# Kernel tuning notes

Measured on AMD Instinct MI355X. Metric: run time of the kernel, lower is better.

## Reference

```python
import jax, jax.numpy as jnp
import numpy as np

BS = 2
EMBED = 256
NH = 8
NL = 4
NP = 4
HD = EMBED // NH
SHAPES = [(128, 128), (64, 64), (32, 32), (16, 16)]
NQ = sum(h * w for h, w in SHAPES)  # 21760


def setup_inputs() -> dict:
    key = jax.random.key(0)
    ks = jax.random.split(key, 12)
    s = 1.0 / np.sqrt(EMBED)
    return {
        "query": jax.random.normal(ks[0], (BS, NQ, EMBED), jnp.float32),
        "reference_points": jax.random.uniform(ks[1], (BS, NQ, NL, 2), jnp.float32),
        "value": jax.random.normal(ks[2], (BS, NQ, EMBED), jnp.float32),
        "W_off": jax.random.normal(ks[3], (EMBED, NH * NL * NP * 2), jnp.float32) * 0.01,
        "b_off": jax.random.normal(ks[4], (NH * NL * NP * 2,), jnp.float32) * 0.5,
        "W_attn": jax.random.normal(ks[5], (EMBED, NH * NL * NP), jnp.float32) * 0.02,
        "b_attn": jnp.zeros((NH * NL * NP,), jnp.float32),
        "W_v": jax.random.normal(ks[6], (EMBED, EMBED), jnp.float32) * s,
        "b_v": jnp.zeros((EMBED,), jnp.float32),
        "W_out": jax.random.normal(ks[7], (EMBED, EMBED), jnp.float32) * s,
        "b_out": jnp.zeros((EMBED,), jnp.float32),
        "value_spatial_shapes": np.asarray(SHAPES, dtype=np.int64),
    }


def _ms_deform_attn(value, shapes, loc, aw):
    # value: [bs,V,nh,d]; loc: [bs,nq,nh,L,P,2] in [0,1]; aw: [bs,nq,nh,L,P]
    bs, V, nh, d = value.shape
    nq = loc.shape[1]
    out = jnp.zeros((bs, nq, nh, d), value.dtype)
    start = 0
    b_idx = jnp.arange(bs)[:, None, None, None]
    h_idx = jnp.arange(nh)[None, None, :, None]
    for l, (H, W) in enumerate(shapes):
        H, W = int(H), int(W)
        v = value[:, start:start + H * W].reshape(bs, H, W, nh, d)
        start += H * W
        g = 2.0 * loc[:, :, :, l] - 1.0  # [bs,nq,nh,P,2], grid_sample convention
        # align_corners=False pixel coordinates
        x = ((g[..., 0] + 1.0) * W - 1.0) * 0.5
        y = ((g[..., 1] + 1.0) * H - 1.0) * 0.5
        x0 = jnp.floor(x); y0 = jnp.floor(y)
        wx1 = x - x0; wx0 = 1.0 - wx1
        wy1 = y - y0; wy0 = 1.0 - wy1

        def gather(yi, xi):
            inb = (yi >= 0) & (yi < H) & (xi >= 0) & (xi < W)
            yc = jnp.clip(yi, 0, H - 1).astype(jnp.int32)
            xc = jnp.clip(xi, 0, W - 1).astype(jnp.int32)
            vals = v[b_idx, yc, xc, h_idx]  # [bs,nq,nh,P,d]
            return vals * inb[..., None].astype(v.dtype)

        samp = (gather(y0, x0) * (wy0 * wx0)[..., None]
                + gather(y0, x0 + 1) * (wy0 * wx1)[..., None]
                + gather(y0 + 1, x0) * (wy1 * wx0)[..., None]
                + gather(y0 + 1, x0 + 1) * (wy1 * wx1)[..., None])
        out = out + jnp.einsum('bqhpd,bqhp->bqhd', samp, aw[:, :, :, l])
    return out.reshape(bs, nq, nh * d)


def reference(query, reference_points, value, W_off, b_off, W_attn, b_attn,
              W_v, b_v, W_out, b_out, value_spatial_shapes):
    shapes = np.asarray(value_spatial_shapes)  # static [L,2]
    bs, nq, _ = query.shape
    v = (value @ W_v + b_v).reshape(bs, -1, NH, HD)
    off = (query @ W_off + b_off).reshape(bs, nq, NH, NL, NP, 2)
    aw = (query @ W_attn + b_attn).reshape(bs, nq, NH, NL * NP)
    aw = jax.nn.softmax(aw, axis=-1).reshape(bs, nq, NH, NL, NP)
    # offset normalizer: (W,H) per level
    norm = jnp.asarray(shapes[:, ::-1].astype(np.float32))  # [L,2]
    loc = reference_points[:, :, None, :, None, :] + off / norm[None, None, None, :, None, :]
    out = _ms_deform_attn(v, shapes, loc, aw)
    return out @ W_out + b_out
```

## Files before the change

### kernel.cpp

```cpp
#include <hip/hip_runtime.h>
#include <math.h>

#define BS 2
#define NQ 21760
#define V_LEN 21760
#define EMBED 256
#define NH 8
#define NL 4
#define NP 4
#define HD 32

typedef __bf16 bf16;
typedef __bf16 bf16x8 __attribute__((ext_vector_type(8)));
typedef __bf16 bf16x4 __attribute__((ext_vector_type(4)));
typedef float f32x4 __attribute__((ext_vector_type(4)));

__global__ __launch_bounds__(256) void cast_wt(const float* __restrict__ W,
                                               bf16* __restrict__ WT, int N)
{
    int id = blockIdx.x * 256 + threadIdx.x;
    int n = id >> 8, k = id & 255;
    WT[id] = (bf16)W[k * N + n];
}

__global__ __launch_bounds__(384) void concat_bias(const float* __restrict__ b_off,
                                                   const float* __restrict__ b_attn,
                                                   float* __restrict__ bc)
{
    int id = threadIdx.x;
    bc[id] = (id < 256) ? b_off[id] : b_attn[id - 256];
}

template<bool A_BF16, bool OUT_BF16>
__global__ __launch_bounds__(256) void gemm_mfma(
    const void* __restrict__ Av, const bf16* __restrict__ WT,
    const float* __restrict__ bias, void* __restrict__ Cv,
    int N, int K, int ntn)
{
    const int bnt = blockIdx.x % ntn;
    const int bmt = blockIdx.x / ntn;
    const int bm = bmt * 128, bn = bnt * 128;

    __shared__ __align__(16) bf16 As[128][40];
    __shared__ __align__(16) bf16 Bs[128][40];

    const int tid = threadIdx.x;
    const int lane = tid & 63, wv = tid >> 6;
    const int wr = wv >> 1, wc = wv & 1;
    const int quad = lane >> 4, l16 = lane & 15;

    f32x4 acc[4][4];
    #pragma unroll
    for (int i = 0; i < 4; i++)
        #pragma unroll
        for (int j = 0; j < 4; j++)
            acc[i][j] = (f32x4){0.f, 0.f, 0.f, 0.f};

    for (int k0 = 0; k0 < K; k0 += 32) {
        if constexpr (A_BF16) {
            const bf16* A = (const bf16*)Av;
            #pragma unroll
            for (int i = 0; i < 2; i++) {
                int row = (tid >> 2) + i * 64, seg = tid & 3;
                bf16x8 v = *(const bf16x8*)&A[(size_t)(bm + row) * K + k0 + seg * 8];
                *(bf16x8*)&As[row][seg * 8] = v;
            }
        } else {
            const float* A = (const float*)Av;
            #pragma unroll
            for (int i = 0; i < 4; i++) {
                int row = (tid >> 3) + i * 32, f4 = tid & 7;
                float4 f = *(const float4*)&A[(size_t)(bm + row) * K + k0 + f4 * 4];
                bf16x4 h;
                h[0] = (bf16)f.x; h[1] = (bf16)f.y; h[2] = (bf16)f.z; h[3] = (bf16)f.w;
                *(bf16x4*)&As[row][f4 * 4] = h;
            }
        }
        #pragma unroll
        for (int i = 0; i < 2; i++) {
            int row = (tid >> 2) + i * 64, seg = tid & 3;
            bf16x8 v = *(const bf16x8*)&WT[(size_t)(bn + row) * K + k0 + seg * 8];
            *(bf16x8*)&Bs[row][seg * 8] = v;
        }
        __syncthreads();

        bf16x8 af[4], bfr[4];
        #pragma unroll
        for (int mi = 0; mi < 4; mi++)
            af[mi] = *(const bf16x8*)&As[wr * 64 + mi * 16 + l16][quad * 8];
        #pragma unroll
        for (int ni = 0; ni < 4; ni++)
            bfr[ni] = *(const bf16x8*)&Bs[wc * 64 + ni * 16 + l16][quad * 8];
        #pragma unroll
        for (int mi = 0; mi < 4; mi++)
            #pragma unroll
            for (int ni = 0; ni < 4; ni++)
                acc[mi][ni] = __builtin_amdgcn_mfma_f32_16x16x32_bf16(
                    af[mi], bfr[ni], acc[mi][ni], 0, 0, 0);
        __syncthreads();
    }

    #pragma unroll
    for (int mi = 0; mi < 4; mi++) {
        #pragma unroll
        for (int ni = 0; ni < 4; ni++) {
            const int col = bn + wc * 64 + ni * 16 + l16;
            const int row0 = bm + wr * 64 + mi * 16 + quad * 4;
            const float bc = bias[col];
            #pragma unroll
            for (int r = 0; r < 4; r++) {
                float v = acc[mi][ni][r] + bc;
                if constexpr (OUT_BF16)
                    ((bf16*)Cv)[(size_t)(row0 + r) * N + col] = (bf16)v;
                else
                    ((float*)Cv)[(size_t)(row0 + r) * N + col] = v;
            }
        }
    }
}

__global__ __launch_bounds__(64) void deform_sample(
    const bf16* __restrict__ vproj, const float* __restrict__ offaw,
    const float* __restrict__ refp, bf16* __restrict__ sampled)
{
    const int q = blockIdx.x;
    const int b = blockIdx.y;
    const int bq = b * NQ + q;
    const int t = threadIdx.x;

    __shared__ float s_off[256];
    __shared__ float s_aw[128];
    __shared__ __align__(16) float s_w[128][4];
    __shared__ __align__(16) int   s_idx[128][4];

    const float* row = offaw + (size_t)bq * 384;
    #pragma unroll
    for (int i = 0; i < 4; i++) s_off[t + i * 64] = row[t + i * 64];
    #pragma unroll
    for (int i = 0; i < 2; i++) s_aw[t + i * 64] = row[256 + t + i * 64];
    __syncthreads();

    if (t < 8) {
        float m = -1e30f;
        #pragma unroll
        for (int i = 0; i < 16; i++) m = fmaxf(m, s_aw[t * 16 + i]);
        float ssum = 0.f;
        #pragma unroll
        for (int i = 0; i < 16; i++) {
            float e = __expf(s_aw[t * 16 + i] - m);
            s_aw[t * 16 + i] = e;
            ssum += e;
        }
        float r = 1.0f / ssum;
        #pragma unroll
        for (int i = 0; i < 16; i++) s_aw[t * 16 + i] *= r;
    }
    __syncthreads();

    #pragma unroll
    for (int sI = 0; sI < 2; sI++) {
        int s = t + sI * 64;
        int h = s >> 4, lp = s & 15, l = lp >> 2, p = lp & 3;
        int Wl = 128 >> l, Hl = 128 >> l;
        int st = (l == 0) ? 0 : (l == 1) ? 16384 : (l == 2) ? 20480 : 21504;
        float rx = refp[((size_t)bq * 4 + l) * 2 + 0];
        float ry = refp[((size_t)bq * 4 + l) * 2 + 1];
        float ox = s_off[((h * NL + l) * NP + p) * 2 + 0];
        float oy = s_off[((h * NL + l) * NP + p) * 2 + 1];
        float fW = (float)Wl, fH = (float)Hl;
        float x = (rx + ox / fW) * fW - 0.5f;
        float y = (ry + oy / fH) * fH - 0.5f;
        float xf = floorf(x), yf = floorf(y);
        int x0 = (int)xf, y0 = (int)yf;
        float wx1 = x - xf, wx0 = 1.f - wx1;
        float wy1 = y - yf, wy0 = 1.f - wy1;
        float aw = s_aw[h * 16 + lp];
        bool vx0 = (x0 >= 0) && (x0 < Wl);
        bool vx1 = (x0 + 1 >= 0) && (x0 + 1 < Wl);
        bool vy0 = (y0 >= 0) && (y0 < Hl);
        bool vy1 = (y0 + 1 >= 0) && (y0 + 1 < Hl);
        int cx0 = min(max(x0, 0), Wl - 1), cx1 = min(max(x0 + 1, 0), Wl - 1);
        int cy0 = min(max(y0, 0), Hl - 1), cy1 = min(max(y0 + 1, 0), Hl - 1);
        int d = lp * 8 + h;
        s_idx[d][0] = st + cy0 * Wl + cx0;  s_w[d][0] = (vy0 && vx0) ? wy0 * wx0 * aw : 0.f;
        s_idx[d][1] = st + cy0 * Wl + cx1;  s_w[d][1] = (vy0 && vx1) ? wy0 * wx1 * aw : 0.f;
        s_idx[d][2] = st + cy1 * Wl + cx0;  s_w[d][2] = (vy1 && vx0) ? wy1 * wx0 * aw : 0.f;
        s_idx[d][3] = st + cy1 * Wl + cx1;  s_w[d][3] = (vy1 && vx1) ? wy1 * wx1 * aw : 0.f;
    }
    __syncthreads();

    const int h = t >> 3;
    const int choff = t * 4;
    const bf16* vbc = vproj + (size_t)b * V_LEN * EMBED + choff;
    float a0 = 0.f, a1 = 0.f, a2 = 0.f, a3 = 0.f;
    #pragma unroll 4
    for (int lp = 0; lp < 16; lp++) {
        const int d = lp * 8 + h;
        const float4 w4 = *(const float4*)&s_w[d][0];
        const int4  i4 = *(const int4*)&s_idx[d][0];
        bf16x4 v0 = *(const bf16x4*)(vbc + (i4.x << 8));
        bf16x4 v1 = *(const bf16x4*)(vbc + (i4.y << 8));
        bf16x4 v2 = *(const bf16x4*)(vbc + (i4.z << 8));
        bf16x4 v3 = *(const bf16x4*)(vbc + (i4.w << 8));
        a0 += w4.x * (float)v0[0] + w4.y * (float)v1[0] + w4.z * (float)v2[0] + w4.w * (float)v3[0];
        a1 += w4.x * (float)v0[1] + w4.y * (float)v1[1] + w4.z * (float)v2[1] + w4.w * (float)v3[1];
        a2 += w4.x * (float)v0[2] + w4.y * (float)v1[2] + w4.z * (float)v2[2] + w4.w * (float)v3[2];
        a3 += w4.x * (float)v0[3] + w4.y * (float)v1[3] + w4.z * (float)v2[3] + w4.w * (float)v3[3];
    }

    bf16x4 o;
    o[0] = (bf16)a0; o[1] = (bf16)a1; o[2] = (bf16)a2; o[3] = (bf16)a3;
    *(bf16x4*)&sampled[(size_t)bq * 256 + choff] = o;
}

extern "C" void kernel_launch(void* const* d_in, const int* in_sizes, int n_in,
                              void* d_out, int out_size, void* d_ws, size_t ws_size,
                              hipStream_t stream)
{
    const float* query  = (const float*)d_in[0];
    const float* refp   = (const float*)d_in[1];
    const float* value  = (const float*)d_in[2];
    const float* W_off  = (const float*)d_in[3];
    const float* b_off  = (const float*)d_in[4];
    const float* W_attn = (const float*)d_in[5];
    const float* b_attn = (const float*)d_in[6];
    const float* W_v    = (const float*)d_in[7];
    const float* b_v    = (const float*)d_in[8];
    const float* W_out  = (const float*)d_in[9];
    const float* b_out  = (const float*)d_in[10];
    float* out = (float*)d_out;

    const int M = BS * NQ;

    char* ws = (char*)d_ws;
    bf16*  WTv   = (bf16*)ws;                      ws += 256 * 256 * 2;
    bf16*  WToa  = (bf16*)ws;                      ws += 384 * 256 * 2;
    bf16*  WTu   = (bf16*)ws;                      ws += 256 * 256 * 2;
    float* bcat  = (float*)ws;                     ws += 384 * 4;
    bf16*  vproj = (bf16*)ws;                      ws += (size_t)M * 256 * 2;
    float* offaw = (float*)ws;                     ws += (size_t)M * 384 * 4;
    bf16*  samp  = (bf16*)ws;                      ws += (size_t)M * 256 * 2;

    cast_wt<<<256, 256, 0, stream>>>(W_v,   WTv, 256);
    cast_wt<<<256, 256, 0, stream>>>(W_off, WToa, 256);
    cast_wt<<<128, 256, 0, stream>>>(W_attn, WToa + 256 * 256, 128);
    cast_wt<<<256, 256, 0, stream>>>(W_out, WTu, 256);
    concat_bias<<<1, 384, 0, stream>>>(b_off, b_attn, bcat);

    gemm_mfma<false, true><<<(M / 128) * 2, 256, 0, stream>>>(value, WTv, b_v, vproj, 256, 256, 2);
    gemm_mfma<false, false><<<(M / 128) * 3, 256, 0, stream>>>(query, WToa, bcat, offaw, 384, 256, 3);
    deform_sample<<<dim3(NQ, BS), dim3(64), 0, stream>>>(vproj, offaw, refp, samp);
    gemm_mfma<true, false><<<(M / 128) * 2, 256, 0, stream>>>(samp, WTu, b_out, out, 256, 256, 2);
}
```

Before: 300.6 us.

## Switch to fp16, fuse prep kernels, retile GEMMs with direct-to-LDS loads, batch deform queries

Merges the weight-cast and bias-concat kernels into one prep launch, and switches intermediates and MFMA from bf16 to fp16. GEMM tiles shrink to 64x128 with a k-major LDS layout, and weight and fp16 A tiles are loaded with global_load_lds. The deform sampler now handles four queries per 256-thread block and precomputes byte offsets, cutting per-block overhead and index math. The fp16 change alters numeric range and precision, and the smaller GEMM tiles reduce data reuse per block.

```diff
diff --git a/kernel.cpp b/kernel.cpp
--- a/kernel.cpp
+++ b/kernel.cpp
@@ -10,108 +10,122 @@
 #define NP 4
 #define HD 32
 
-typedef __bf16 bf16;
-typedef __bf16 bf16x8 __attribute__((ext_vector_type(8)));
-typedef __bf16 bf16x4 __attribute__((ext_vector_type(4)));
+typedef _Float16 f16;
+typedef _Float16 half8 __attribute__((ext_vector_type(8)));
+typedef _Float16 half4v __attribute__((ext_vector_type(4)));
 typedef float f32x4 __attribute__((ext_vector_type(4)));
 
-__global__ __launch_bounds__(256) void cast_wt(const float* __restrict__ W,
-                                               bf16* __restrict__ WT, int N)
-{
-    int id = blockIdx.x * 256 + threadIdx.x;
-    int n = id >> 8, k = id & 255;
-    WT[id] = (bf16)W[k * N + n];
-}
-
-__global__ __launch_bounds__(384) void concat_bias(const float* __restrict__ b_off,
-                                                   const float* __restrict__ b_attn,
-                                                   float* __restrict__ bc)
-{
-    int id = threadIdx.x;
-    bc[id] = (id < 256) ? b_off[id] : b_attn[id - 256];
-}
-
-template<bool A_BF16, bool OUT_BF16>
+__device__ __forceinline__ void load_lds16(const void* g, void* l) {
+    __builtin_amdgcn_global_load_lds(
+        (const __attribute__((address_space(1))) void*)g,
+        (__attribute__((address_space(3))) void*)l, 16, 0, 0);
+}
+
+__global__ __launch_bounds__(256) void prep(
+    const float* __restrict__ W_v, const float* __restrict__ W_off,
+    const float* __restrict__ W_attn, const float* __restrict__ W_out,
+    const float* __restrict__ b_off, const float* __restrict__ b_attn,
+    f16* __restrict__ WTv, f16* __restrict__ WToa, f16* __restrict__ WTu,
+    float* __restrict__ bcat)
+{
+    const int nb = blockIdx.x;
+    const int k = threadIdx.x;
+    if (nb < 256) {
+        WTv[nb * 256 + k] = (f16)W_v[k * 256 + nb];
+    } else if (nb < 640) {
+        int j = nb - 256;
+        float w = (j < 256) ? W_off[k * 256 + j] : W_attn[k * 128 + (j - 256)];
+        WToa[j * 256 + k] = (f16)w;
+    } else if (nb < 896) {
+        int j = nb - 640;
+        WTu[j * 256 + k] = (f16)W_out[k * 256 + j];
+    } else if (nb == 896) {
+        bcat[k] = b_off[k];
+        if (k < 128) bcat[256 + k] = b_attn[k];
+    }
+}
+
+template<bool AF16, bool OUTF16>
 __global__ __launch_bounds__(256) void gemm_mfma(
-    const void* __restrict__ Av, const bf16* __restrict__ WT,
+    const void* __restrict__ Av, const f16* __restrict__ WT,
     const float* __restrict__ bias, void* __restrict__ Cv,
-    int N, int K, int ntn)
+    int N, int ntn)
 {
     const int bnt = blockIdx.x % ntn;
     const int bmt = blockIdx.x / ntn;
-    const int bm = bmt * 128, bn = bnt * 128;
-
-    __shared__ __align__(16) bf16 As[128][40];
-    __shared__ __align__(16) bf16 Bs[128][40];
+    const int bm = bmt * 64, bn = bnt * 128;
+    const int K = 256;
+
+    __shared__ __align__(16) f16 As[4 * 64 * 8];
+    __shared__ __align__(16) f16 Bs[4 * 128 * 8];
 
     const int tid = threadIdx.x;
     const int lane = tid & 63, wv = tid >> 6;
-    const int wr = wv >> 1, wc = wv & 1;
     const int quad = lane >> 4, l16 = lane & 15;
 
-    f32x4 acc[4][4];
+    f32x4 acc[4][2];
     #pragma unroll
     for (int i = 0; i < 4; i++)
         #pragma unroll
-        for (int j = 0; j < 4; j++)
+        for (int j = 0; j < 2; j++)
             acc[i][j] = (f32x4){0.f, 0.f, 0.f, 0.f};
 
     for (int k0 = 0; k0 < K; k0 += 32) {
-        if constexpr (A_BF16) {
-            const bf16* A = (const bf16*)Av;
-            #pragma unroll
-            for (int i = 0; i < 2; i++) {
-                int row = (tid >> 2) + i * 64, seg = tid & 3;
-                bf16x8 v = *(const bf16x8*)&A[(size_t)(bm + row) * K + k0 + seg * 8];
-                *(bf16x8*)&As[row][seg * 8] = v;
-            }
+        #pragma unroll
+        for (int i = 0; i < 2; i++) {
+            int S0 = (i * 4 + wv) * 64;
+            int S = S0 + lane;
+            int col = S & 127, kcg = S >> 7;
+            load_lds16(&WT[(size_t)(bn + col) * K + k0 + kcg * 8], &Bs[S0 * 8]);
+        }
+        if constexpr (AF16) {
+            const f16* A = (const f16*)Av;
+            int S0 = wv * 64;
+            int S = S0 + lane;
+            int row = S & 63, kcg = S >> 6;
+            load_lds16(&A[(size_t)(bm + row) * K + k0 + kcg * 8], &As[S0 * 8]);
         } else {
             const float* A = (const float*)Av;
             #pragma unroll
-            for (int i = 0; i < 4; i++) {
-                int row = (tid >> 3) + i * 32, f4 = tid & 7;
-                float4 f = *(const float4*)&A[(size_t)(bm + row) * K + k0 + f4 * 4];
-                bf16x4 h;
-                h[0] = (bf16)f.x; h[1] = (bf16)f.y; h[2] = (bf16)f.z; h[3] = (bf16)f.w;
-                *(bf16x4*)&As[row][f4 * 4] = h;
+            for (int i = 0; i < 2; i++) {
+                int F = i * 256 + tid;
+                int row = F >> 3, kq = F & 7;
+                float4 f = *(const float4*)&A[(size_t)(bm + row) * K + k0 + kq * 4];
+                half4v h;
+                h[0] = (f16)f.x; h[1] = (f16)f.y; h[2] = (f16)f.z; h[3] = (f16)f.w;
+                *(half4v*)&As[((kq >> 1) * 64 + row) * 8 + (kq & 1) * 4] = h;
             }
         }
-        #pragma unroll
-        for (int i = 0; i < 2; i++) {
-            int row = (tid >> 2) + i * 64, seg = tid & 3;
-            bf16x8 v = *(const bf16x8*)&WT[(size_t)(bn + row) * K + k0 + seg * 8];
-            *(bf16x8*)&Bs[row][seg * 8] = v;
-        }
         __syncthreads();
 
-        bf16x8 af[4], bfr[4];
+        half8 af[4], bf[2];
         #pragma unroll
         for (int mi = 0; mi < 4; mi++)
-            af[mi] = *(const bf16x8*)&As[wr * 64 + mi * 16 + l16][quad * 8];
-        #pragma unroll
-        for (int ni = 0; ni < 4; ni++)
-            bfr[ni] = *(const bf16x8*)&Bs[wc * 64 + ni * 16 + l16][quad * 8];
+            af[mi] = *(const half8*)&As[(quad * 64 + mi * 16 + l16) * 8];
+        #pragma unroll
+        for (int ni = 0; ni < 2; ni++)
+            bf[ni] = *(const half8*)&Bs[(quad * 128 + wv * 32 + ni * 16 + l16) * 8];
         #pragma unroll
         for (int mi = 0; mi < 4; mi++)
             #pragma unroll
-            for (int ni = 0; ni < 4; ni++)
-                acc[mi][ni] = __builtin_amdgcn_mfma_f32_16x16x32_bf16(
-                    af[mi], bfr[ni], acc[mi][ni], 0, 0, 0);
+            for (int ni = 0; ni < 2; ni++)
+                acc[mi][ni] = __builtin_amdgcn_mfma_f32_16x16x32_f16(
+                    af[mi], bf[ni], acc[mi][ni], 0, 0, 0);
         __syncthreads();
     }
 
     #pragma unroll
     for (int mi = 0; mi < 4; mi++) {
         #pragma unroll
-        for (int ni = 0; ni < 4; ni++) {
-            const int col = bn + wc * 64 + ni * 16 + l16;
-            const int row0 = bm + wr * 64 + mi * 16 + quad * 4;
+        for (int ni = 0; ni < 2; ni++) {
+            const int col = bn + wv * 32 + ni * 16 + l16;
+            const int row0 = bm + mi * 16 + quad * 4;
             const float bc = bias[col];
             #pragma unroll
             for (int r = 0; r < 4; r++) {
                 float v = acc[mi][ni][r] + bc;
-                if constexpr (OUT_BF16)
-                    ((bf16*)Cv)[(size_t)(row0 + r) * N + col] = (bf16)v;
+                if constexpr (OUTF16)
+                    ((f16*)Cv)[(size_t)(row0 + r) * N + col] = (f16)v;
                 else
                     ((float*)Cv)[(size_t)(row0 + r) * N + col] = v;
             }
@@ -119,98 +133,98 @@
     }
 }
 
-__global__ __launch_bounds__(64) void deform_sample(
-    const bf16* __restrict__ vproj, const float* __restrict__ offaw,
-    const float* __restrict__ refp, bf16* __restrict__ sampled)
-{
-    const int q = blockIdx.x;
+__global__ __launch_bounds__(256) void deform_sample(
+    const f16* __restrict__ vproj, const float* __restrict__ offaw,
+    const float* __restrict__ refp, f16* __restrict__ sampled)
+{
+    const int wv = threadIdx.x >> 6;
+    const int lane = threadIdx.x & 63;
+    const int q = blockIdx.x * 4 + wv;
     const int b = blockIdx.y;
     const int bq = b * NQ + q;
-    const int t = threadIdx.x;
-
-    __shared__ float s_off[256];
-    __shared__ float s_aw[128];
-    __shared__ __align__(16) float s_w[128][4];
-    __shared__ __align__(16) int   s_idx[128][4];
+
+    __shared__ float s_off[4][256];
+    __shared__ float s_aw[4][128];
+    __shared__ __align__(16) float s_w[4][128][4];
+    __shared__ __align__(16) int   s_idx[4][128][4];
 
     const float* row = offaw + (size_t)bq * 384;
     #pragma unroll
-    for (int i = 0; i < 4; i++) s_off[t + i * 64] = row[t + i * 64];
-    #pragma unroll
-    for (int i = 0; i < 2; i++) s_aw[t + i * 64] = row[256 + t + i * 64];
+    for (int i = 0; i < 4; i++) s_off[wv][lane + i * 64] = row[lane + i * 64];
+    #pragma unroll
+    for (int i = 0; i < 2; i++) s_aw[wv][lane + i * 64] = row[256 + lane + i * 64];
     __syncthreads();
 
-    if (t < 8) {
+    if (lane < 8) {
         float m = -1e30f;
         #pragma unroll
-        for (int i = 0; i < 16; i++) m = fmaxf(m, s_aw[t * 16 + i]);
+        for (int i = 0; i < 16; i++) m = fmaxf(m, s_aw[wv][lane * 16 + i]);
         float ssum = 0.f;
         #pragma unroll
         for (int i = 0; i < 16; i++) {
-            float e = __expf(s_aw[t * 16 + i] - m);
-            s_aw[t * 16 + i] = e;
+            float e = __expf(s_aw[wv][lane * 16 + i] - m);
+            s_aw[wv][lane * 16 + i] = e;
             ssum += e;
         }
         float r = 1.0f / ssum;
         #pragma unroll
-        for (int i = 0; i < 16; i++) s_aw[t * 16 + i] *= r;
+        for (int i = 0; i < 16; i++) s_aw[wv][lane * 16 + i] *= r;
     }
     __syncthreads();
 
     #pragma unroll
     for (int sI = 0; sI < 2; sI++) {
-        int s = t + sI * 64;
-        int h = s >> 4, lp = s & 15, l = lp >> 2, p = lp & 3;
-        int Wl = 128 >> l, Hl = 128 >> l;
+        int d = lane + sI * 64;
+        int h = d & 7, lp = d >> 3, l = lp >> 2, p = lp & 3;
+        int Wl = 128 >> l;
         int st = (l == 0) ? 0 : (l == 1) ? 16384 : (l == 2) ? 20480 : 21504;
-        float rx = refp[((size_t)bq * 4 + l) * 2 + 0];
-        float ry = refp[((size_t)bq * 4 + l) * 2 + 1];
-        float ox = s_off[((h * NL + l) * NP + p) * 2 + 0];
-        float oy = s_off[((h * NL + l) * NP + p) * 2 + 1];
-        float fW = (float)Wl, fH = (float)Hl;
+        float rx = refp[(size_t)bq * 8 + l * 2 + 0];
+        float ry = refp[(size_t)bq * 8 + l * 2 + 1];
+        float ox = s_off[wv][((h * NL + l) * NP + p) * 2 + 0];
+        float oy = s_off[wv][((h * NL + l) * NP + p) * 2 + 1];
+        float fW = (float)Wl;
         float x = (rx + ox / fW) * fW - 0.5f;
-        float y = (ry + oy / fH) * fH - 0.5f;
+        float y = (ry + oy / fW) * fW - 0.5f;
         float xf = floorf(x), yf = floorf(y);
         int x0 = (int)xf, y0 = (int)yf;
         float wx1 = x - xf, wx0 = 1.f - wx1;
         float wy1 = y - yf, wy0 = 1.f - wy1;
-        float aw = s_aw[h * 16 + lp];
+        float aw = s_aw[wv][h * 16 + lp];
         bool vx0 = (x0 >= 0) && (x0 < Wl);
         bool vx1 = (x0 + 1 >= 0) && (x0 + 1 < Wl);
-        bool vy0 = (y0 >= 0) && (y0 < Hl);
-        bool vy1 = (y0 + 1 >= 0) && (y0 + 1 < Hl);
+        bool vy0 = (y0 >= 0) && (y0 < Wl);
+        bool vy1 = (y0 + 1 >= 0) && (y0 + 1 < Wl);
         int cx0 = min(max(x0, 0), Wl - 1), cx1 = min(max(x0 + 1, 0), Wl - 1);
-        int cy0 = min(max(y0, 0), Hl - 1), cy1 = min(max(y0 + 1, 0), Hl - 1);
-        int d = lp * 8 + h;
-        s_idx[d][0] = st + cy0 * Wl + cx0;  s_w[d][0] = (vy0 && vx0) ? wy0 * wx0 * aw : 0.f;
-        s_idx[d][1] = st + cy0 * Wl + cx1;  s_w[d][1] = (vy0 && vx1) ? wy0 * wx1 * aw : 0.f;
-        s_idx[d][2] = st + cy1 * Wl + cx0;  s_w[d][2] = (vy1 && vx0) ? wy1 * wx0 * aw : 0.f;
-        s_idx[d][3] = st + cy1 * Wl + cx1;  s_w[d][3] = (vy1 && vx1) ? wy1 * wx1 * aw : 0.f;
+        int cy0 = min(max(y0, 0), Wl - 1), cy1 = min(max(y0 + 1, 0), Wl - 1);
+        s_idx[wv][d][0] = (st + cy0 * Wl + cx0) << 9;  s_w[wv][d][0] = (vy0 && vx0) ? wy0 * wx0 * aw : 0.f;
+        s_idx[wv][d][1] = (st + cy0 * Wl + cx1) << 9;  s_w[wv][d][1] = (vy0 && vx1) ? wy0 * wx1 * aw : 0.f;
+        s_idx[wv][d][2] = (st + cy1 * Wl + cx0) << 9;  s_w[wv][d][2] = (vy1 && vx0) ? wy1 * wx0 * aw : 0.f;
+        s_idx[wv][d][3] = (st + cy1 * Wl + cx1) << 9;  s_w[wv][d][3] = (vy1 && vx1) ? wy1 * wx1 * aw : 0.f;
     }
     __syncthreads();
 
-    const int h = t >> 3;
-    const int choff = t * 4;
-    const bf16* vbc = vproj + (size_t)b * V_LEN * EMBED + choff;
+    const int h = lane >> 3;
+    const unsigned int cb = (unsigned int)lane * 8u;
+    const char* vb = (const char*)(vproj + (size_t)b * V_LEN * EMBED);
     float a0 = 0.f, a1 = 0.f, a2 = 0.f, a3 = 0.f;
     #pragma unroll 4
     for (int lp = 0; lp < 16; lp++) {
         const int d = lp * 8 + h;
-        const float4 w4 = *(const float4*)&s_w[d][0];
-        const int4  i4 = *(const int4*)&s_idx[d][0];
-        bf16x4 v0 = *(const bf16x4*)(vbc + (i4.x << 8));
-        bf16x4 v1 = *(const bf16x4*)(vbc + (i4.y << 8));
-        bf16x4 v2 = *(const bf16x4*)(vbc + (i4.z << 8));
-        bf16x4 v3 = *(const bf16x4*)(vbc + (i4.w << 8));
+        const float4 w4 = *(const float4*)&s_w[wv][d][0];
+        const int4  i4 = *(const int4*)&s_idx[wv][d][0];
+        half4v v0 = *(const half4v*)(vb + ((unsigned int)i4.x + cb));
+        half4v v1 = *(const half4v*)(vb + ((unsigned int)i4.y + cb));
+        half4v v2 = *(const half4v*)(vb + ((unsigned int)i4.z + cb));
+        half4v v3 = *(const half4v*)(vb + ((unsigned int)i4.w + cb));
         a0 += w4.x * (float)v0[0] + w4.y * (float)v1[0] + w4.z * (float)v2[0] + w4.w * (float)v3[0];
         a1 += w4.x * (float)v0[1] + w4.y * (float)v1[1] + w4.z * (float)v2[1] + w4.w * (float)v3[1];
         a2 += w4.x * (float)v0[2] + w4.y * (float)v1[2] + w4.z * (float)v2[2] + w4.w * (float)v3[2];
         a3 += w4.x * (float)v0[3] + w4.y * (float)v1[3] + w4.z * (float)v2[3] + w4.w * (float)v3[3];
     }
 
-    bf16x4 o;
-    o[0] = (bf16)a0; o[1] = (bf16)a1; o[2] = (bf16)a2; o[3] = (bf16)a3;
-    *(bf16x4*)&sampled[(size_t)bq * 256 + choff] = o;
+    half4v o;
+    o[0] = (f16)a0; o[1] = (f16)a1; o[2] = (f16)a2; o[3] = (f16)a3;
+    *(half4v*)&sampled[(size_t)bq * 256 + lane * 4] = o;
 }
 
 extern "C" void kernel_launch(void* const* d_in, const int* in_sizes, int n_in,
@@ -233,22 +247,18 @@
     const int M = BS * NQ;
 
     char* ws = (char*)d_ws;
-    bf16*  WTv   = (bf16*)ws;                      ws += 256 * 256 * 2;
-    bf16*  WToa  = (bf16*)ws;                      ws += 384 * 256 * 2;
-    bf16*  WTu   = (bf16*)ws;                      ws += 256 * 256 * 2;
-    float* bcat  = (float*)ws;                     ws += 384 * 4;
-    bf16*  vproj = (bf16*)ws;                      ws += (size_t)M * 256 * 2;
-    float* offaw = (float*)ws;                     ws += (size_t)M * 384 * 4;
-    bf16*  samp  = (bf16*)ws;                      ws += (size_t)M * 256 * 2;
-
-    cast_wt<<<256, 256, 0, stream>>>(W_v,   WTv, 256);
-    cast_wt<<<256, 256, 0, stream>>>(W_off, WToa, 256);
-    cast_wt<<<128, 256, 0, stream>>>(W_attn, WToa + 256 * 256, 128);
-    cast_wt<<<256, 256, 0, stream>>>(W_out, WTu, 256);
-    concat_bias<<<1, 384, 0, stream>>>(b_off, b_attn, bcat);
-
-    gemm_mfma<false, true><<<(M / 128) * 2, 256, 0, stream>>>(value, WTv, b_v, vproj, 256, 256, 2);
-    gemm_mfma<false, false><<<(M / 128) * 3, 256, 0, stream>>>(query, WToa, bcat, offaw, 384, 256, 3);
-    deform_sample<<<dim3(NQ, BS), dim3(64), 0, stream>>>(vproj, offaw, refp, samp);
-    gemm_mfma<true, false><<<(M / 128) * 2, 256, 0, stream>>>(samp, WTu, b_out, out, 256, 256, 2);
-}
+    f16*   WTv   = (f16*)ws;    ws += 256 * 256 * 2;
+    f16*   WToa  = (f16*)ws;    ws += 384 * 256 * 2;
+    f16*   WTu   = (f16*)ws;    ws += 256 * 256 * 2;
+    float* bcat  = (float*)ws;  ws += 384 * 4 + 128;
+    f16*   vproj = (f16*)ws;    ws += (size_t)M * 256 * 2;
+    float* offaw = (float*)ws;  ws += (size_t)M * 384 * 4;
+    f16*   samp  = (f16*)ws;    ws += (size_t)M * 256 * 2;
+
+    prep<<<897, 256, 0, stream>>>(W_v, W_off, W_attn, W_out, b_off, b_attn,
+                                  WTv, WToa, WTu, bcat);
+    gemm_mfma<false, true><<<(M / 64) * 2, 256, 0, stream>>>(value, WTv, b_v, vproj, 256, 2);
+    gemm_mfma<false, false><<<(M / 64) * 3, 256, 0, stream>>>(query, WToa, bcat, offaw, 384, 3);
+    deform_sample<<<dim3(NQ / 4, BS), 256, 0, stream>>>(vproj, offaw, refp, samp);
+    gemm_mfma<true, false><<<(M / 64) * 2, 256, 0, stream>>>(samp, WTu, b_out, out, 256, 2);
+}
```

Result: slower. 331.0 us (+10.1%).
